# Kernel tuning notes

Measured on AMD Instinct MI355X. Metric: run time of the kernel, lower is better.

The kernel has to match this reference:

```python
import jax, jax.numpy as jnp
import numpy as np
import math

TAU = 0.5        # module stores self.tau = 1.0 / tau with tau=2.0
THRESHOLD = 1.0
SURR_C = 1.0 / (2.0 * math.sqrt(2.0 * math.pi))  # coefficient in Stochastic.backward


@jax.custom_vjp
def spike(v):
    # Stochastic.forward: (input > 0).float()
    return (v > 0).astype(v.dtype)


def _spike_fwd(v):
    return spike(v), v


def _spike_bwd(v, g):
    # Stochastic.backward: grad * 1/(2*sqrt(2*pi)) * exp(-v^2/2)
    return (g * (SURR_C * jnp.exp(-0.5 * v * v)),)


spike.defvjp(_spike_fwd, _spike_bwd)


def setup_inputs() -> dict:
    key = jax.random.key(0)
    x = jax.random.normal(key, (32, 128, 8192), dtype=jnp.float32)  # [B, T, N]
    return {"x": x}


def reference(x):
    # Eval-mode iterative stochastic-LIF update (no noise injection).
    xt = jnp.swapaxes(x, 0, 1)  # [T, B, N] for scan over time

    def step(u, x_t):
        u = TAU * u + x_t                # leaky integrate
        o = spike(u - THRESHOLD)         # fire
        u = u * (1.0 - o)                # hard reset by multiply
        return u, o

    u0 = jnp.zeros_like(xt[0])
    _, o = jax.lax.scan(step, u0, xt)
    return jnp.swapaxes(o, 0, 1)  # [B, T, N]
```

## Files before the change

kernel.cpp:

```cpp
#include <hip/hip_runtime.h>


constexpr int B = 32;
constexpr int T = 128;
constexpr int N = 8192;

__global__ __launch_bounds__(256) void lif_kernel(const float* __restrict__ x,
                                                  float* __restrict__ out) {
    int idx = blockIdx.x * blockDim.x + threadIdx.x;
    int b = idx >> 13;
    int n = idx & (N - 1);
    size_t base = (size_t)b * T * N + n;
    const float* xp = x   + base;
    float*       op = out + base;

    float u = 0.f;
    #pragma unroll 8
    for (int t = 0; t < T; ++t) {
        float xt = xp[(size_t)t * N];
        u = 0.5f * u + xt;
        float o = (u > 1.0f) ? 1.0f : 0.0f;
        u = (u > 1.0f) ? 0.0f : u;
        op[(size_t)t * N] = o;
    }
}

extern "C" void kernel_launch(void* const* d_in, const int* in_sizes, int n_in,
                              void* d_out, int out_size, void* d_ws, size_t ws_size,
                              hipStream_t stream) {
    const float* x  = (const float*)d_in[0];
    float*      out = (float*)d_out;
    int total = B * N;
    lif_kernel<<<total / 256, 256, 0, stream>>>(x, out);
}
```

Baseline: 236.5 us.

## Double-buffer time chunks into LDS with async global-to-LDS 16-byte loads

Each block now prefetches a 16-timestep chunk of 256 neurons into shared memory using global_load_lds 16-byte async copies. It double-buffers so that chunk c+1 is in flight while chunk c is integrated serially. The aim is more memory-level parallelism and less exposed load latency in the serial per-neuron time scan, which with only 1024 blocks is latency-bound. The cost is extra LDS traffic and a block-wide barrier per chunk. Correctness also relies on the barrier waiting for the async LDS loads to complete.

```diff
diff --git a/kernel.cpp b/kernel.cpp
--- a/kernel.cpp
+++ b/kernel.cpp
@@ -1,27 +1,64 @@
 #include <hip/hip_runtime.h>
+#include <stdint.h>
 
 
-constexpr int B = 32;
-constexpr int T = 128;
-constexpr int N = 8192;
+constexpr int B   = 32;
+constexpr int T   = 128;
+constexpr int N   = 8192;
+constexpr int N4  = N / 4;
+constexpr int TC  = 16;
+constexpr int NC  = T / TC;
+constexpr int NW4 = 64;
 
-__global__ __launch_bounds__(256) void lif_kernel(const float* __restrict__ x,
+__device__ __forceinline__ void async16(void* lds_dst, const void* g_src) {
+    __builtin_amdgcn_global_load_lds(
+        (const __attribute__((address_space(1))) void*)g_src,
+        (__attribute__((address_space(3))) void*)lds_dst, 16, 0, 0);
+}
+
+__global__ __launch_bounds__(256) void lif_kernel(const float4* __restrict__ x,
                                                   float* __restrict__ out) {
-    int idx = blockIdx.x * blockDim.x + threadIdx.x;
-    int b = idx >> 13;
-    int n = idx & (N - 1);
-    size_t base = (size_t)b * T * N + n;
-    const float* xp = x   + base;
-    float*       op = out + base;
+    __shared__ float4 buf[2][TC][NW4];
+
+    const int tid   = threadIdx.x;
+    const int wave  = tid >> 6;
+    const int lane  = tid & 63;
+    const int b     = blockIdx.x >> 5;
+    const int ntile = blockIdx.x & 31;
+    const size_t xbase4 = (size_t)b * T * N4 + (size_t)ntile * NW4;
+    const size_t obase  = (size_t)b * T * N  + (size_t)ntile * (NW4 * 4) + tid;
+
+    {
+        const float4* g0 = x + xbase4;
+        #pragma unroll
+        for (int k = 0; k < TC / 4; ++k) {
+            const int t_sub = k * 4 + wave;
+            async16(&buf[0][t_sub][lane], g0 + (size_t)t_sub * N4 + lane);
+        }
+    }
 
     float u = 0.f;
-    #pragma unroll 8
-    for (int t = 0; t < T; ++t) {
-        float xt = xp[(size_t)t * N];
-        u = 0.5f * u + xt;
-        float o = (u > 1.0f) ? 1.0f : 0.0f;
-        u = (u > 1.0f) ? 0.0f : u;
-        op[(size_t)t * N] = o;
+    #pragma unroll
+    for (int c = 0; c < NC; ++c) {
+        __syncthreads();
+        if (c + 1 < NC) {
+            const float4* g = x + xbase4 + (size_t)(c + 1) * TC * N4;
+            #pragma unroll
+            for (int k = 0; k < TC / 4; ++k) {
+                const int t_sub = k * 4 + wave;
+                async16(&buf[(c + 1) & 1][t_sub][lane], g + (size_t)t_sub * N4 + lane);
+            }
+        }
+        const float* lb = (const float*)buf[c & 1];
+        float* op = out + obase + (size_t)c * TC * N;
+        #pragma unroll
+        for (int t = 0; t < TC; ++t) {
+            const float xt = lb[t * 256 + tid];
+            u = 0.5f * u + xt;
+            const float o = (u > 1.0f) ? 1.0f : 0.0f;
+            u = (u > 1.0f) ? 0.0f : u;
+            op[(size_t)t * N] = o;
+        }
     }
 }
 
@@ -30,6 +67,6 @@
                               hipStream_t stream) {
     const float* x  = (const float*)d_in[0];
     float*      out = (float*)d_out;
-    int total = B * N;
-    lif_kernel<<<total / 256, 256, 0, stream>>>(x, out);
+    const int nblocks = B * (N / (NW4 * 4));
+    lif_kernel<<<nblocks, 256, 0, stream>>>((const float4*)x, out);
 }
```

Result: no change. 232.2 us (-1.8%).

## Double-buffer time chunks into LDS with async global-to-LDS loads

Applied to the files above, without the earlier changes.

The LIF scan is restructured so each 64-thread block handles one batch row and a 64-wide slice of neurons. Input for 16 timesteps at a time is prefetched straight into a double-buffered LDS tile with global_load_lds, so the next chunk's loads overlap with the serial recurrence on the current chunk. The aim is to keep more memory requests in flight than the old per-thread unroll-8 loop allowed. In exchange it adds a block barrier per chunk, and correctness depends on the async LDS writes having completed before they are read.

```diff
diff --git a/kernel.cpp b/kernel.cpp
--- a/kernel.cpp
+++ b/kernel.cpp
@@ -1,27 +1,54 @@
 #include <hip/hip_runtime.h>
 
 
-constexpr int B = 32;
-constexpr int T = 128;
-constexpr int N = 8192;
+constexpr int B  = 32;
+constexpr int T  = 128;
+constexpr int N  = 8192;
+constexpr int NW = 64;
+constexpr int TC = 16;
+constexpr int NC = T / TC;
 
-__global__ __launch_bounds__(256) void lif_kernel(const float* __restrict__ x,
-                                                  float* __restrict__ out) {
-    int idx = blockIdx.x * blockDim.x + threadIdx.x;
-    int b = idx >> 13;
-    int n = idx & (N - 1);
-    size_t base = (size_t)b * T * N + n;
-    const float* xp = x   + base;
-    float*       op = out + base;
+__device__ __forceinline__ void async4(void* lds_dst, const void* g_src) {
+    __builtin_amdgcn_global_load_lds(
+        (const __attribute__((address_space(1))) void*)g_src,
+        (__attribute__((address_space(3))) void*)lds_dst, 4, 0, 0);
+}
+
+__global__ __launch_bounds__(64) void lif_kernel(const float* __restrict__ x,
+                                                 float* __restrict__ out) {
+    __shared__ float buf[2][TC][NW];
+
+    const int tid   = threadIdx.x;
+    const int b     = blockIdx.x >> 7;
+    const int ntile = blockIdx.x & 127;
+    const size_t base = (size_t)b * T * N + (size_t)ntile * NW;
+    const float* xp = x + base;
+    float*       op = out + base + tid;
+
+    #pragma unroll
+    for (int j = 0; j < TC; ++j)
+        async4(&buf[0][j][tid], xp + (size_t)j * N + tid);
 
     float u = 0.f;
-    #pragma unroll 8
-    for (int t = 0; t < T; ++t) {
-        float xt = xp[(size_t)t * N];
-        u = 0.5f * u + xt;
-        float o = (u > 1.0f) ? 1.0f : 0.0f;
-        u = (u > 1.0f) ? 0.0f : u;
-        op[(size_t)t * N] = o;
+    #pragma unroll
+    for (int c = 0; c < NC; ++c) {
+        __syncthreads();
+        if (c + 1 < NC) {
+            const float* g = xp + (size_t)(c + 1) * TC * N;
+            #pragma unroll
+            for (int j = 0; j < TC; ++j)
+                async4(&buf[(c + 1) & 1][j][tid], g + (size_t)j * N + tid);
+        }
+        const float* lb = &buf[c & 1][0][0];
+        float* o = op + (size_t)c * TC * N;
+        #pragma unroll
+        for (int t = 0; t < TC; ++t) {
+            const float xt = lb[t * NW + tid];
+            u = 0.5f * u + xt;
+            const float sp = (u > 1.0f) ? 1.0f : 0.0f;
+            u = (u > 1.0f) ? 0.0f : u;
+            o[(size_t)t * N] = sp;
+        }
     }
 }
 
@@ -30,6 +57,6 @@
                               hipStream_t stream) {
     const float* x  = (const float*)d_in[0];
     float*      out = (float*)d_out;
-    int total = B * N;
-    lif_kernel<<<total / 256, 256, 0, stream>>>(x, out);
+    const int nblocks = B * (N / NW);
+    lif_kernel<<<nblocks, NW, 0, stream>>>(x, out);
 }
```

Result: no change. 239.3 us (+1.2%).
